# Kernel optimization log

Hardware: AMD Instinct MI355X
Metric: run time of the kernel (lower is better)

Reference implementation:

```python
import jax, jax.numpy as jnp
import numpy as np

B, L = 256, 100
N100, N10_100, N0_10 = 40000, 80000, 120000
D100, D10_100, D0_10 = 500, 250, 250  # layers[0]/2, layers[0]/4, remainder
H1, H2 = 200, 1000                    # layers = [1000, 200, 1000]
NUM_PIX = N100 + N10_100 + N0_10


def setup_inputs() -> dict:
    key = jax.random.key(0)
    ks = jax.random.split(key, 11)
    rn = lambda k, shape, scale: jax.random.normal(k, shape, jnp.float32) * scale
    return {
        'songs_bucket': jax.random.randint(ks[0], (B, L), 0, 3, jnp.int32),
        'songs_id': jax.random.randint(ks[1], (B, L), 0, N100, jnp.int32),
        'W100': rn(ks[2], (N100, D100), 0.02),
        'W10_100': rn(ks[3], (N10_100, D10_100), 0.02),
        'W0_10': rn(ks[4], (N0_10, D0_10), 0.02),
        'fc1_w': rn(ks[5], (H1, 1000), 0.03),
        'fc1_b': jnp.zeros((H1,), jnp.float32),
        'fc2_w': rn(ks[6], (H2, H1), 0.07),
        'fc2_b': jnp.zeros((H2,), jnp.float32),
        'out_w': rn(ks[7], (NUM_PIX, H2), 0.03),
        'out_b': jnp.zeros((NUM_PIX,), jnp.float32),
    }


def _masked_mean(table, ids, mask):
    # table: [V, D], ids: [B, L], mask: [B, L] bool -> [B, D]
    emb = table[ids]                                   # gather [B, L, D]
    m = mask.astype(emb.dtype)
    ssum = jnp.einsum('bl,bld->bd', m, emb)            # masked segment-sum
    cnt = m.sum(axis=1)                                # [B]
    mean = ssum / jnp.maximum(cnt, 1.0)[:, None]
    return jnp.where(cnt[:, None] > 0, mean, 0.0)     # empty bucket -> zeros


def reference(songs_bucket, songs_id, W100, W10_100, W0_10,
              fc1_w, fc1_b, fc2_w, fc2_b, out_w, out_b):
    # per-bucket masked embedding mean (vectorized embedding-bag)
    e0 = _masked_mean(W100, songs_id, songs_bucket == 0)       # [B, 500]
    e1 = _masked_mean(W10_100, songs_id, songs_bucket == 1)    # [B, 250]
    e2 = _masked_mean(W0_10, songs_id, songs_bucket == 2)      # [B, 250]
    x = jnp.concatenate([e0, e1, e2], axis=-1)                 # [B, 1000]
    # tiny MLP (dropout p=False -> p=0, a no-op)
    h = jax.nn.relu(x @ fc1_w.T + fc1_b)                       # [B, 200]
    h = jax.nn.relu(h @ fc2_w.T + fc2_b)                       # [B, 1000]
    ratings = h @ out_w.T + out_b                              # [B, NUM_PIX]
    return ratings
```

## Files before the change

kernel.cpp:

```cpp
#include <hip/hip_runtime.h>

#define NUM_B 256
#define SEQ_L 100
#define NPIX  240000
#define KPAD  1024
#define BN    128
#define BK    128
#define NWG   1875

typedef __attribute__((ext_vector_type(8))) short short8;
typedef __attribute__((ext_vector_type(4))) float f32x4;

static __device__ __forceinline__ unsigned short f2bf(float f) {
  unsigned int u = __builtin_bit_cast(unsigned int, f);
  u += 0x7fffu + ((u >> 16) & 1u);
  return (unsigned short)(u >> 16);
}

__global__ __launch_bounds__(1024) void embed_mlp_kernel(
    const int* __restrict__ bucket, const int* __restrict__ ids,
    const float* __restrict__ W100, const float* __restrict__ W10,
    const float* __restrict__ W0,
    const float* __restrict__ fc1_w, const float* __restrict__ fc1_b,
    const float* __restrict__ fc2_w, const float* __restrict__ fc2_b,
    unsigned short* __restrict__ h2out)
{
  __shared__ __align__(16) float xw[16][1000];
  __shared__ __align__(16) float xs[1000];
  __shared__ __align__(16) float h1s[200];
  __shared__ int sb[SEQ_L], sid[SEQ_L];
  __shared__ int cnt[16][3];
  __shared__ int cntT[3];

  const int row = blockIdx.x, tid = threadIdx.x;
  const int wid = tid >> 6, lane = tid & 63;

  if (tid < SEQ_L) {
    sb[tid]  = bucket[row * SEQ_L + tid];
    sid[tid] = ids[row * SEQ_L + tid];
  }
  __syncthreads();

  float acc0[8] = {0,0,0,0,0,0,0,0};
  float acc1[4] = {0,0,0,0};
  float acc2[4] = {0,0,0,0};
  int c0 = 0, c1 = 0, c2 = 0;

  for (int l = wid; l < SEQ_L; l += 16) {
    const int b = sb[l];
    const long id = sid[l];
    if (b == 0) {
      ++c0; const float* r = W100 + id * 500;
      #pragma unroll
      for (int j = 0; j < 7; ++j) acc0[j] += r[lane + 64 * j];
      if (lane < 52) acc0[7] += r[lane + 448];
    } else if (b == 1) {
      ++c1; const float* r = W10 + id * 250;
      #pragma unroll
      for (int j = 0; j < 3; ++j) acc1[j] += r[lane + 64 * j];
      if (lane < 58) acc1[3] += r[lane + 192];
    } else {
      ++c2; const float* r = W0 + id * 250;
      #pragma unroll
      for (int j = 0; j < 3; ++j) acc2[j] += r[lane + 64 * j];
      if (lane < 58) acc2[3] += r[lane + 192];
    }
  }
  {
    float* xp = xw[wid];
    #pragma unroll
    for (int j = 0; j < 8; ++j) { int d = lane + 64 * j; if (d < 500) xp[d] = acc0[j]; }
    #pragma unroll
    for (int j = 0; j < 4; ++j) { int d = lane + 64 * j; if (d < 250) xp[500 + d] = acc1[j]; }
    #pragma unroll
    for (int j = 0; j < 4; ++j) { int d = lane + 64 * j; if (d < 250) xp[750 + d] = acc2[j]; }
    if (lane == 0) { cnt[wid][0] = c0; cnt[wid][1] = c1; cnt[wid][2] = c2; }
  }
  __syncthreads();
  if (tid < 3) { int s = 0; for (int w = 0; w < 16; ++w) s += cnt[w][tid]; cntT[tid] = s; }
  __syncthreads();
  if (tid < 1000) {
    float s = 0.f;
    #pragma unroll
    for (int w = 0; w < 16; ++w) s += xw[w][tid];
    const int bkt = tid < 500 ? 0 : (tid < 750 ? 1 : 2);
    const int c = cntT[bkt];
    xs[tid] = c ? s / (float)c : 0.f;
  }
  __syncthreads();

  const int g = tid >> 4, sl = tid & 15;

  for (int o = g; o < 200; o += 64) {
    const f32x4* wr = (const f32x4*)(fc1_w + o * 1000);
    const f32x4* xv = (const f32x4*)xs;
    float p = 0.f;
    for (int j = sl; j < 250; j += 16) {
      f32x4 a = xv[j], b = wr[j];
      p += a.x * b.x + a.y * b.y + a.z * b.z + a.w * b.w;
    }
    #pragma unroll
    for (int off = 8; off; off >>= 1) p += __shfl_down(p, off, 16);
    if (sl == 0) h1s[o] = fmaxf(p + fc1_b[o], 0.f);
  }
  __syncthreads();

  unsigned short* hrow = h2out + (long)row * KPAD;
  for (int o = g; o < 1000; o += 64) {
    const f32x4* wr = (const f32x4*)(fc2_w + o * 200);
    const f32x4* hv = (const f32x4*)h1s;
    float p = 0.f;
    #pragma unroll
    for (int j = sl; j < 50; j += 16) {
      f32x4 a = hv[j], b = wr[j];
      p += a.x * b.x + a.y * b.y + a.z * b.z + a.w * b.w;
    }
    #pragma unroll
    for (int off = 8; off; off >>= 1) p += __shfl_down(p, off, 16);
    if (sl == 0) hrow[o] = f2bf(fmaxf(p + fc2_b[o], 0.f));
  }
  if (tid < KPAD - 1000) hrow[1000 + tid] = 0;
}

__global__ __launch_bounds__(512) void out_gemm_kernel(
    const unsigned short* __restrict__ h2,
    const float* __restrict__ out_w,
    const float* __restrict__ out_b,
    float* __restrict__ out)
{
  __shared__ __align__(16) unsigned char lds[98304];
  unsigned char* As = lds;
  unsigned char* Bs = lds + 65536;

  const int tid = threadIdx.x;

  const int q = NWG / 8, r = NWG % 8;
  const int xcd = blockIdx.x & 7, bidx = blockIdx.x >> 3;
  const int wg = (xcd < r ? xcd * (q + 1) : r * (q + 1) + (xcd - r) * q) + bidx;
  const long n0 = (long)wg * BN;

  const f32x4 fz = {0.f, 0.f, 0.f, 0.f};

  f32x4 bReg[8];

  auto dmaA = [&](int kt) {
    #pragma unroll
    for (int i = 0; i < 8; ++i) {
      const int c = tid + 512 * i;
      const int rw = c >> 4;
      const int k16s = (c & 15) ^ (rw & 7);
      const unsigned short* src = h2 + rw * KPAD + kt * BK + k16s * 8;
      __builtin_amdgcn_global_load_lds(
          (const __attribute__((address_space(1))) void*)src,
          (__attribute__((address_space(3))) void*)(As + c * 16),
          16, 0, 0);
    }
  };
  auto loadB = [&](int k0) {
    #pragma unroll
    for (int i = 0; i < 8; ++i) {
      int c = tid + 512 * i;
      int n = c >> 5, qq = c & 31;
      int k = k0 + qq * 4;
      bReg[i] = (k < 1000)
        ? __builtin_nontemporal_load((const f32x4*)(out_w + (long)(n0 + n) * 1000 + k))
        : fz;
    }
  };
  auto storeB = [&]() {
    #pragma unroll
    for (int i = 0; i < 8; ++i) {
      int c = tid + 512 * i;
      int n = c >> 5, qq = c & 31;
      ushort4 h;
      h.x = f2bf(bReg[i].x); h.y = f2bf(bReg[i].y);
      h.z = f2bf(bReg[i].z); h.w = f2bf(bReg[i].w);
      *(ushort4*)(Bs + n * 256 + ((qq * 8) ^ ((n & 7) << 4))) = h;
    }
  };

  const int wid = tid >> 6, lane = tid & 63;
  const int wm = wid >> 2, wn = wid & 3;
  const int lrow = lane & 15, lkg = lane >> 4;

  f32x4 acc[8][2];
  #pragma unroll
  for (int m = 0; m < 8; ++m) { acc[m][0] = fz; acc[m][1] = fz; }

  dmaA(0); loadB(0);
  #pragma unroll 1
  for (int kt = 0; kt < 8; ++kt) {
    storeB();
    __syncthreads();
    if (kt < 7) loadB((kt + 1) * BK);
    #pragma unroll
    for (int kk = 0; kk < 4; ++kk) {
      short8 bf[2];
      #pragma unroll
      for (int n = 0; n < 2; ++n) {
        int nr = wn * 32 + n * 16 + lrow;
        bf[n] = *(const short8*)(Bs + nr * 256 + (((kk * 64) + lkg * 16) ^ ((nr & 7) << 4)));
      }
      #pragma unroll
      for (int m = 0; m < 8; ++m) {
        int rr = wm * 128 + m * 16 + lrow;
        short8 af = *(const short8*)(As + rr * 256 + (((kk * 64) + lkg * 16) ^ ((rr & 7) << 4)));
        acc[m][0] = __builtin_amdgcn_mfma_f32_16x16x32_bf16(af, bf[0], acc[m][0], 0, 0, 0);
        acc[m][1] = __builtin_amdgcn_mfma_f32_16x16x32_bf16(af, bf[1], acc[m][1], 0, 0, 0);
      }
    }
    asm volatile("s_waitcnt lgkmcnt(0)" ::: "memory");
    __builtin_amdgcn_s_barrier();
    __builtin_amdgcn_sched_barrier(0);
    if (kt < 7) dmaA(kt + 1);
  }

  const float b0 = out_b[n0 + wn * 32 + lrow];
  const float b1 = out_b[n0 + wn * 32 + 16 + lrow];
  float* E = (float*)lds;
  #pragma unroll
  for (int half = 0; half < 2; ++half) {
    __syncthreads();
    if (wm == half) {
      #pragma unroll
      for (int m = 0; m < 8; ++m) {
        #pragma unroll
        for (int n = 0; n < 2; ++n) {
          const int col = wn * 32 + n * 16 + lrow;
          const float bias = n ? b1 : b0;
          #pragma unroll
          for (int rr = 0; rr < 4; ++rr) {
            const int rowl = m * 16 + lkg * 4 + rr;
            E[rowl * 132 + col] = acc[m][n][rr] + bias;
          }
        }
      }
    }
    __syncthreads();
    const int rbase = half * 128;
    #pragma unroll
    for (int s = 0; s < 8; ++s) {
      const int rowl = s * 16 + (tid >> 5);
      const int c = (tid & 31) * 4;
      f32x4 v = *(const f32x4*)(E + rowl * 132 + c);
      __builtin_nontemporal_store(v, (f32x4*)(out + (long)(rbase + rowl) * NPIX + n0 + c));
    }
  }
}

extern "C" void kernel_launch(void* const* d_in, const int* in_sizes, int n_in,
                              void* d_out, int out_size, void* d_ws, size_t ws_size,
                              hipStream_t stream) {
  const int*   bucket = (const int*)d_in[0];
  const int*   ids    = (const int*)d_in[1];
  const float* W100   = (const float*)d_in[2];
  const float* W10    = (const float*)d_in[3];
  const float* W0     = (const float*)d_in[4];
  const float* fc1w   = (const float*)d_in[5];
  const float* fc1b   = (const float*)d_in[6];
  const float* fc2w   = (const float*)d_in[7];
  const float* fc2b   = (const float*)d_in[8];
  const float* outw   = (const float*)d_in[9];
  const float* outb   = (const float*)d_in[10];
  float* out = (float*)d_out;
  unsigned short* h2w = (unsigned short*)d_ws;

  embed_mlp_kernel<<<NUM_B, 1024, 0, stream>>>(bucket, ids, W100, W10, W0,
                                               fc1w, fc1b, fc2w, fc2b, h2w);
  out_gemm_kernel<<<NWG, 512, 0, stream>>>(h2w, outw, outb, out);
}
```

Measured before the change: 319.3 us.

## Load out_w fragments directly into registers, drop B LDS staging

The output GEMM no longer stages the fp32 out_w tile through registers and LDS. Each lane now loads its MFMA B fragment straight from global memory and converts it to bf16 in registers. This shrinks LDS use so more workgroups can be resident (launch bounds set to 4), and removes the B store/sync step. In exchange the global loads are no longer prefetched a tile ahead and are less coalesced, and the lanes sharing a row load it again, so memory latency sits directly in the MFMA loop.

```diff
diff --git a/kernel.cpp b/kernel.cpp
--- a/kernel.cpp
+++ b/kernel.cpp
@@ -122,15 +122,14 @@
   if (tid < KPAD - 1000) hrow[1000 + tid] = 0;
 }
 
-__global__ __launch_bounds__(512) void out_gemm_kernel(
+__global__ __launch_bounds__(512, 4) void out_gemm_kernel(
     const unsigned short* __restrict__ h2,
     const float* __restrict__ out_w,
     const float* __restrict__ out_b,
     float* __restrict__ out)
 {
-  __shared__ __align__(16) unsigned char lds[98304];
+  __shared__ __align__(16) unsigned char lds[69632];
   unsigned char* As = lds;
-  unsigned char* Bs = lds + 65536;
 
   const int tid = threadIdx.x;
 
@@ -138,10 +137,6 @@
   const int xcd = blockIdx.x & 7, bidx = blockIdx.x >> 3;
   const int wg = (xcd < r ? xcd * (q + 1) : r * (q + 1) + (xcd - r) * q) + bidx;
   const long n0 = (long)wg * BN;
-
-  const f32x4 fz = {0.f, 0.f, 0.f, 0.f};
-
-  f32x4 bReg[8];
 
   auto dmaA = [&](int kt) {
     #pragma unroll
@@ -156,59 +151,51 @@
           16, 0, 0);
     }
   };
-  auto loadB = [&](int k0) {
-    #pragma unroll
-    for (int i = 0; i < 8; ++i) {
-      int c = tid + 512 * i;
-      int n = c >> 5, qq = c & 31;
-      int k = k0 + qq * 4;
-      bReg[i] = (k < 1000)
-        ? __builtin_nontemporal_load((const f32x4*)(out_w + (long)(n0 + n) * 1000 + k))
-        : fz;
-    }
-  };
-  auto storeB = [&]() {
-    #pragma unroll
-    for (int i = 0; i < 8; ++i) {
-      int c = tid + 512 * i;
-      int n = c >> 5, qq = c & 31;
-      ushort4 h;
-      h.x = f2bf(bReg[i].x); h.y = f2bf(bReg[i].y);
-      h.z = f2bf(bReg[i].z); h.w = f2bf(bReg[i].w);
-      *(ushort4*)(Bs + n * 256 + ((qq * 8) ^ ((n & 7) << 4))) = h;
-    }
-  };
 
   const int wid = tid >> 6, lane = tid & 63;
   const int wm = wid >> 2, wn = wid & 3;
   const int lrow = lane & 15, lkg = lane >> 4;
 
+  const f32x4 fz = {0.f, 0.f, 0.f, 0.f};
   f32x4 acc[8][2];
   #pragma unroll
   for (int m = 0; m < 8; ++m) { acc[m][0] = fz; acc[m][1] = fz; }
 
-  dmaA(0); loadB(0);
-  #pragma unroll 1
-  for (int kt = 0; kt < 8; ++kt) {
-    storeB();
-    __syncthreads();
-    if (kt < 7) loadB((kt + 1) * BK);
+  const float* Bp[2];
+  #pragma unroll
+  for (int n = 0; n < 2; ++n)
+    Bp[n] = out_w + (n0 + wn * 32 + n * 16 + lrow) * 1000 + lkg * 8;
+
+  auto compute = [&](int kt) {
     #pragma unroll
     for (int kk = 0; kk < 4; ++kk) {
       short8 bf[2];
       #pragma unroll
       for (int n = 0; n < 2; ++n) {
-        int nr = wn * 32 + n * 16 + lrow;
-        bf[n] = *(const short8*)(Bs + nr * 256 + (((kk * 64) + lkg * 16) ^ ((nr & 7) << 4)));
+        int k = kt * BK + kk * 32;
+        const float* p = (k + lkg * 8 < 1000) ? (Bp[n] + k) : (Bp[n] - lkg * 8);
+        f32x4 lo = *(const f32x4*)p;
+        f32x4 hi = *(const f32x4*)(p + 4);
+        bf[n][0] = (short)f2bf(lo.x); bf[n][1] = (short)f2bf(lo.y);
+        bf[n][2] = (short)f2bf(lo.z); bf[n][3] = (short)f2bf(lo.w);
+        bf[n][4] = (short)f2bf(hi.x); bf[n][5] = (short)f2bf(hi.y);
+        bf[n][6] = (short)f2bf(hi.z); bf[n][7] = (short)f2bf(hi.w);
       }
       #pragma unroll
       for (int m = 0; m < 8; ++m) {
-        int rr = wm * 128 + m * 16 + lrow;
+        const int rr = wm * 128 + m * 16 + lrow;
         short8 af = *(const short8*)(As + rr * 256 + (((kk * 64) + lkg * 16) ^ ((rr & 7) << 4)));
         acc[m][0] = __builtin_amdgcn_mfma_f32_16x16x32_bf16(af, bf[0], acc[m][0], 0, 0, 0);
         acc[m][1] = __builtin_amdgcn_mfma_f32_16x16x32_bf16(af, bf[1], acc[m][1], 0, 0, 0);
       }
     }
+  };
+
+  dmaA(0);
+  #pragma unroll 1
+  for (int kt = 0; kt < 8; ++kt) {
+    __syncthreads();
+    compute(kt);
     asm volatile("s_waitcnt lgkmcnt(0)" ::: "memory");
     __builtin_amdgcn_s_barrier();
     __builtin_amdgcn_sched_barrier(0);
```

Result: slower. 527.2 us (+65.1%).
